# Optimization experiments

Hardware: AMD Instinct MI355X
Metric: run time of the kernel (lower is better)

The kernel has to match this reference:

```python
import jax, jax.numpy as jnp
import numpy as np

IN_DIM, HIDDEN_DIM, OUT_DIM = 128, 256, 128
N_NODES, N_EDGES = 100000, 1000000


def setup_inputs() -> dict:
    key = jax.random.key(0)
    ks = jax.random.split(key, 8)
    s = lambda d: 1.0 / np.sqrt(d)
    x = jax.random.normal(ks[0], (N_NODES, IN_DIM), dtype=jnp.float32)
    edge_index = jax.random.randint(ks[1], (2, N_EDGES), 0, N_NODES, dtype=jnp.int64)
    # encoder: Linear(in,hid) -> ReLU -> Linear(hid,out)
    W1 = jax.random.uniform(ks[2], (IN_DIM, HIDDEN_DIM), jnp.float32, -s(IN_DIM), s(IN_DIM))
    b1 = jnp.zeros((HIDDEN_DIM,), jnp.float32)
    W2 = jax.random.uniform(ks[3], (HIDDEN_DIM, OUT_DIM), jnp.float32, -s(HIDDEN_DIM), s(HIDDEN_DIM))
    b2 = jnp.zeros((OUT_DIM,), jnp.float32)
    # pred: Linear(2*out,hid) -> ReLU -> Linear(hid,1)
    W3 = jax.random.uniform(ks[4], (2 * OUT_DIM, HIDDEN_DIM), jnp.float32, -s(2 * OUT_DIM), s(2 * OUT_DIM))
    b3 = jnp.zeros((HIDDEN_DIM,), jnp.float32)
    W4 = jax.random.uniform(ks[5], (HIDDEN_DIM, 1), jnp.float32, -s(HIDDEN_DIM), s(HIDDEN_DIM))
    b4 = jnp.zeros((1,), jnp.float32)
    return {"x": x, "edge_index": edge_index, "W1": W1, "b1": b1, "W2": W2,
            "b2": b2, "W3": W3, "b3": b3, "W4": W4, "b4": b4}


def reference(x, edge_index, W1, b1, W2, b2, W3, b3, W4, b4):
    # node encoder
    h = jax.nn.relu(x @ W1 + b1) @ W2 + b2            # [N, out_dim]
    # edge gather + concat
    h_src = h[edge_index[0]]                          # [E, out_dim]
    h_dst = h[edge_index[1]]                          # [E, out_dim]
    e = jnp.concatenate([h_src, h_dst], axis=-1)      # [E, 2*out_dim]
    # edge predictor
    logits = jax.nn.relu(e @ W3 + b3) @ W4 + b4       # [E, 1]
    return jax.nn.sigmoid(logits)
```

## Files before the change

### kernel.cpp

```cpp
#include <hip/hip_runtime.h>


#define NN 100000
#define NE 1000000
#define NTN 1563
#define GRID_N 256
#define GRID_EP 1024

typedef __attribute__((ext_vector_type(8))) __bf16 bf16x8;
typedef __attribute__((ext_vector_type(4))) float f32x4;
typedef __attribute__((ext_vector_type(4))) unsigned short us4;

__device__ __forceinline__ unsigned short f2bf(float f) {
    unsigned u = __float_as_uint(f);
    return (unsigned short)((u + 0x7FFFu + ((u >> 16) & 1u)) >> 16);
}
__device__ __forceinline__ float bflo(unsigned w) {
    return __uint_as_float(w << 16);
}
__device__ __forceinline__ float bfhi(unsigned w) {
    return __uint_as_float(w & 0xffff0000u);
}

template <int CTRL>
__device__ __forceinline__ float dpp_add(float v) {
    return v + __int_as_float(__builtin_amdgcn_update_dpp(
                   0, __float_as_int(v), CTRL, 0xF, 0xF, true));
}
__device__ __forceinline__ float row_reduce16(float v) {
    v = dpp_add<0x118>(v);
    v = dpp_add<0x114>(v);
    v = dpp_add<0x112>(v);
    v = dpp_add<0x111>(v);
    return v;
}

__global__ void prep1(const float* __restrict__ W1, const float* __restrict__ W2,
                      const float* __restrict__ W3, const float* __restrict__ b2,
                      const float* __restrict__ b3, const void* __restrict__ eidx,
                      unsigned short* __restrict__ w1s, float* __restrict__ wutf,
                      float* __restrict__ wvtf, float* __restrict__ bu,
                      float* __restrict__ bv, int* __restrict__ flag) {
    int t = blockIdx.x * blockDim.x + threadIdx.x;
    if (t < 32768) {
        int k = t >> 8, n = t & 255;
        w1s[(k >> 3) * 2048 + n * 8 + (k & 7)] = f2bf(W1[t]);
    }
    if (t < 65536) {
        int k = t >> 8, n = t & 255;
        float s = 0.0f;
        for (int j = 0; j < 128; ++j) s += W2[k * 128 + j] * W3[j * 256 + n];
        wutf[t] = s;
    } else {
        int i = t - 65536;
        int k = i >> 8, n = i & 255;
        float s = 0.0f;
        for (int j = 0; j < 128; ++j) s += W2[k * 128 + j] * W3[(128 + j) * 256 + n];
        wvtf[i] = s;
    }
    if (t < 256) {
        float s = b3[t];
        for (int j = 0; j < 128; ++j) s += b2[j] * W3[j * 256 + t];
        bu[t] = s;
    } else if (t < 512) {
        int n = t - 256;
        float s = 0.0f;
        for (int j = 0; j < 128; ++j) s += b2[j] * W3[(128 + j) * 256 + n];
        bv[n] = s;
    }
    if (t == 0) {
        const unsigned* u = (const unsigned*)eidx;
        int all0 = 1;
        for (int i = 0; i < 32; ++i) all0 &= (u[2 * i + 1] == 0u);
        *flag = all0;
    }
}

__global__ void prep2(const float* __restrict__ wutf, const float* __restrict__ wvtf,
                      unsigned short* __restrict__ wuts, unsigned short* __restrict__ wvts) {
    int t = blockIdx.x * blockDim.x + threadIdx.x;
    if (t < 65536) {
        int k = t >> 8, n = t & 255;
        wuts[(k >> 3) * 2048 + n * 8 + (k & 7)] = f2bf(wutf[t]);
    } else {
        int i = t - 65536;
        int k = i >> 8, n = i & 255;
        wvts[(k >> 3) * 2048 + n * 8 + (k & 7)] = f2bf(wvtf[i]);
    }
}

__global__ __launch_bounds__(512, 2) void node_uv(
    const float* __restrict__ x, const float* __restrict__ b1,
    const unsigned short* __restrict__ w1s, const unsigned short* __restrict__ wuts,
    const unsigned short* __restrict__ wvts, const float* __restrict__ bu,
    const float* __restrict__ bv, unsigned short* __restrict__ Ug,
    unsigned short* __restrict__ Vg) {
    __shared__ __align__(16) unsigned short A1[64 * 136];
    __shared__ __align__(16) unsigned short A2[64 * 264];

    const int t = threadIdx.x, lane = t & 63, w = t >> 6;
    const int cl = lane & 15, q = lane >> 4;
    const int nb = w * 32;

    bf16x8 wutr[8][2], wvtr[8][2];
#pragma unroll
    for (int s = 0; s < 8; ++s)
#pragma unroll
        for (int nt = 0; nt < 2; ++nt) {
            wutr[s][nt] = *(const bf16x8*)(wuts + (s * 4 + q) * 2048 +
                                           (nb + nt * 16 + cl) * 8);
            wvtr[s][nt] = *(const bf16x8*)(wvts + (s * 4 + q) * 2048 +
                                           (nb + nt * 16 + cl) * 8);
        }
    float b1v[2], buv[2], bvv[2];
#pragma unroll
    for (int nt = 0; nt < 2; ++nt) {
        int n = nb + nt * 16 + cl;
        b1v[nt] = b1[n];
        buv[nt] = bu[n];
        bvv[nt] = bv[n];
    }

    for (int tile = blockIdx.x; tile < NTN; tile += GRID_N) {
        const int m0 = tile * 64;
        {
            const float4* x4 = (const float4*)x;
#pragma unroll
            for (int i = 0; i < 4; ++i) {
                int lin = i * 512 + t;
                int m = lin >> 5, c = lin & 31;
                int node = m0 + m;
                if (node > NN - 1) node = NN - 1;
                float4 v = x4[node * 32 + c];
                us4 b;
                b.x = f2bf(v.x); b.y = f2bf(v.y); b.z = f2bf(v.z); b.w = f2bf(v.w);
                *(us4*)(A1 + m * 136 + c * 4) = b;
            }
        }
        __syncthreads();

        f32x4 acc[4][2];
#pragma unroll
        for (int mt = 0; mt < 4; ++mt)
#pragma unroll
            for (int nt = 0; nt < 2; ++nt)
                acc[mt][nt] = (f32x4){b1v[nt], b1v[nt], b1v[nt], b1v[nt]};
#pragma unroll
        for (int s = 0; s < 4; ++s) {
            bf16x8 a[4], bw[2];
#pragma unroll
            for (int mt = 0; mt < 4; ++mt)
                a[mt] = *(const bf16x8*)(A1 + (mt * 16 + cl) * 136 + s * 32 + q * 8);
#pragma unroll
            for (int nt = 0; nt < 2; ++nt)
                bw[nt] = *(const bf16x8*)(w1s + (s * 4 + q) * 2048 +
                                          (nb + nt * 16 + cl) * 8);
#pragma unroll
            for (int mt = 0; mt < 4; ++mt)
#pragma unroll
                for (int nt = 0; nt < 2; ++nt)
                    acc[mt][nt] = __builtin_amdgcn_mfma_f32_16x16x32_bf16(
                        a[mt], bw[nt], acc[mt][nt], 0, 0, 0);
        }
#pragma unroll
        for (int mt = 0; mt < 4; ++mt)
#pragma unroll
            for (int nt = 0; nt < 2; ++nt)
#pragma unroll
                for (int r = 0; r < 4; ++r) {
                    float v = fmaxf(acc[mt][nt][r], 0.0f);
                    A2[(mt * 16 + q * 4 + r) * 264 + nb + nt * 16 + cl] = f2bf(v);
                }
        __syncthreads();

        f32x4 accU[4][2], accV[4][2];
#pragma unroll
        for (int mt = 0; mt < 4; ++mt)
#pragma unroll
            for (int nt = 0; nt < 2; ++nt) {
                accU[mt][nt] = (f32x4){buv[nt], buv[nt], buv[nt], buv[nt]};
                accV[mt][nt] = (f32x4){bvv[nt], bvv[nt], bvv[nt], bvv[nt]};
            }
#pragma unroll
        for (int s = 0; s < 8; ++s) {
            bf16x8 a[4];
#pragma unroll
            for (int mt = 0; mt < 4; ++mt)
                a[mt] = *(const bf16x8*)(A2 + (mt * 16 + cl) * 264 + s * 32 + q * 8);
#pragma unroll
            for (int mt = 0; mt < 4; ++mt)
#pragma unroll
                for (int nt = 0; nt < 2; ++nt) {
                    accU[mt][nt] = __builtin_amdgcn_mfma_f32_16x16x32_bf16(
                        a[mt], wutr[s][nt], accU[mt][nt], 0, 0, 0);
                    accV[mt][nt] = __builtin_amdgcn_mfma_f32_16x16x32_bf16(
                        a[mt], wvtr[s][nt], accV[mt][nt], 0, 0, 0);
                }
        }
#pragma unroll
        for (int mt = 0; mt < 4; ++mt)
#pragma unroll
            for (int nt = 0; nt < 2; ++nt)
#pragma unroll
                for (int r = 0; r < 4; ++r) {
                    int node = m0 + mt * 16 + q * 4 + r;
                    if (node < NN) {
                        int col = nb + nt * 16 + cl;
                        Ug[node * 256 + col] = f2bf(accU[mt][nt][r]);
                        Vg[node * 256 + col] = f2bf(accV[mt][nt][r]);
                    }
                }
    }
}

#define TERM(uw, vw, wa, wb)                                     \
    (fmaxf(bflo(uw) + bflo(vw), 0.0f) * (wa) +                   \
     fmaxf(bfhi(uw) + bfhi(vw), 0.0f) * (wb))

__global__ __launch_bounds__(256, 4) void edge_pred(
    const void* __restrict__ eidx, const unsigned short* __restrict__ Ut,
    const unsigned short* __restrict__ Vt, const float* __restrict__ W4,
    const float* __restrict__ b4, const int* __restrict__ flag,
    float* __restrict__ out) {
    const int t = threadIdx.x, lane = t & 63;
    const int cl = lane & 15, g = lane >> 4;
    const int gwid = (blockIdx.x * 256 + t) >> 6;
    const int nw = (GRID_EP * 256) >> 6;
    const bool i64f = (*flag != 0);
    const int* ei32 = (const int*)eidx;
    const long long* ei64 = (const long long*)eidx;

    float w4a[8], w4b[8];
#pragma unroll
    for (int j = 0; j < 8; ++j) {
        w4a[j] = W4[cl * 8 + j];
        w4b[j] = W4[128 + cl * 8 + j];
    }
    const float b4v = b4[0];

    for (int base = gwid * 8; base < NE; base += nw * 8) {
        const int eA = base + g, eB = base + 4 + g;
        int sA = i64f ? (int)ei64[eA] : ei32[eA];
        int dA = i64f ? (int)ei64[NE + eA] : ei32[NE + eA];
        int sB = i64f ? (int)ei64[eB] : ei32[eB];
        int dB = i64f ? (int)ei64[NE + eB] : ei32[NE + eB];
        sA = sA < 0 ? 0 : (sA > NN - 1 ? NN - 1 : sA);
        dA = dA < 0 ? 0 : (dA > NN - 1 ? NN - 1 : dA);
        sB = sB < 0 ? 0 : (sB > NN - 1 ? NN - 1 : sB);
        dB = dB < 0 ? 0 : (dB > NN - 1 ? NN - 1 : dB);

        const uint4* ua = (const uint4*)(Ut + (long)sA * 256) + cl;
        const uint4* va = (const uint4*)(Vt + (long)dA * 256) + cl;
        const uint4* ub = (const uint4*)(Ut + (long)sB * 256) + cl;
        const uint4* vb = (const uint4*)(Vt + (long)dB * 256) + cl;
        uint4 ua0 = ua[0], ua1 = ua[16];
        uint4 va0 = va[0], va1 = va[16];
        uint4 ub0 = ub[0], ub1 = ub[16];
        uint4 vb0 = vb[0], vb1 = vb[16];

        float accA =
            TERM(ua0.x, va0.x, w4a[0], w4a[1]) + TERM(ua0.y, va0.y, w4a[2], w4a[3]) +
            TERM(ua0.z, va0.z, w4a[4], w4a[5]) + TERM(ua0.w, va0.w, w4a[6], w4a[7]) +
            TERM(ua1.x, va1.x, w4b[0], w4b[1]) + TERM(ua1.y, va1.y, w4b[2], w4b[3]) +
            TERM(ua1.z, va1.z, w4b[4], w4b[5]) + TERM(ua1.w, va1.w, w4b[6], w4b[7]);
        float accB =
            TERM(ub0.x, vb0.x, w4a[0], w4a[1]) + TERM(ub0.y, vb0.y, w4a[2], w4a[3]) +
            TERM(ub0.z, vb0.z, w4a[4], w4a[5]) + TERM(ub0.w, vb0.w, w4a[6], w4a[7]) +
            TERM(ub1.x, vb1.x, w4b[0], w4b[1]) + TERM(ub1.y, vb1.y, w4b[2], w4b[3]) +
            TERM(ub1.z, vb1.z, w4b[4], w4b[5]) + TERM(ub1.w, vb1.w, w4b[6], w4b[7]);

        accA = row_reduce16(accA);
        accB = row_reduce16(accB);
        if (cl == 15) {
            out[eA] = 1.0f / (1.0f + __expf(-(accA + b4v)));
            out[eB] = 1.0f / (1.0f + __expf(-(accB + b4v)));
        }
    }
}

extern "C" void kernel_launch(void* const* d_in, const int* in_sizes, int n_in,
                              void* d_out, int out_size, void* d_ws, size_t ws_size,
                              hipStream_t stream) {
    const float* x  = (const float*)d_in[0];
    const void*  ei = d_in[1];
    const float* W1 = (const float*)d_in[2];
    const float* b1 = (const float*)d_in[3];
    const float* W2 = (const float*)d_in[4];
    const float* b2 = (const float*)d_in[5];
    const float* W3 = (const float*)d_in[6];
    const float* b3 = (const float*)d_in[7];
    const float* W4 = (const float*)d_in[8];
    const float* b4 = (const float*)d_in[9];

    char* ws = (char*)d_ws;
    int* flag            = (int*)ws;
    unsigned short* w1s  = (unsigned short*)(ws + 256);
    unsigned short* wuts = (unsigned short*)(ws + 65792);
    unsigned short* wvts = (unsigned short*)(ws + 196864);
    float* bu            = (float*)(ws + 327936);
    float* bv            = (float*)(ws + 328960);
    float* wutf          = (float*)(ws + 329984);
    float* wvtf          = (float*)(ws + 592128);
    unsigned short* Ug   = (unsigned short*)(ws + 1048576);
    unsigned short* Vg   = (unsigned short*)(ws + 52248576);

    prep1<<<512, 256, 0, stream>>>(W1, W2, W3, b2, b3, ei, w1s, wutf, wvtf, bu, bv, flag);
    prep2<<<512, 256, 0, stream>>>(wutf, wvtf, wuts, wvts);
    node_uv<<<GRID_N, 512, 0, stream>>>(x, b1, w1s, wuts, wvts, bu, bv, Ug, Vg);
    edge_pred<<<GRID_EP, 256, 0, stream>>>(ei, Ug, Vg, W4, b4, flag, (float*)d_out);
}
```

Baseline: 328.1 us.

## Fuse weight prep kernels, use one-tile-per-block node encoder, enlarge edge grid

The prep2 kernel is merged into prep1 so the folded W2·W3 weights are written directly in bf16 swizzled layout, removing one launch and an fp32 round trip. node_uv moves from a persistent 256-block grid of 512 threads, which kept the U/V weights in registers, to one 64-node tile per 256-thread block. Each wave now covers 64 columns and the U and V GEMMs run in two sequential passes with weights streamed from global memory. The edge predictor grid is doubled and its launch bound raised to 8 blocks per CU for more occupancy, at the cost of register pressure and extra weight reloads per tile.

After: 331.8 us. No clear change (+1.1%).

```diff
diff --git a/kernel.cpp b/kernel.cpp
--- a/kernel.cpp
+++ b/kernel.cpp
@@ -4,8 +4,7 @@
 #define NN 100000
 #define NE 1000000
 #define NTN 1563
-#define GRID_N 256
-#define GRID_EP 1024
+#define GRID_EP 2048
 
 typedef __attribute__((ext_vector_type(8))) __bf16 bf16x8;
 typedef __attribute__((ext_vector_type(4))) float f32x4;
@@ -38,8 +37,9 @@
 __global__ void prep1(const float* __restrict__ W1, const float* __restrict__ W2,
                       const float* __restrict__ W3, const float* __restrict__ b2,
                       const float* __restrict__ b3, const void* __restrict__ eidx,
-                      unsigned short* __restrict__ w1s, float* __restrict__ wutf,
-                      float* __restrict__ wvtf, float* __restrict__ bu,
+                      unsigned short* __restrict__ w1s,
+                      unsigned short* __restrict__ wuts,
+                      unsigned short* __restrict__ wvts, float* __restrict__ bu,
                       float* __restrict__ bv, int* __restrict__ flag) {
     int t = blockIdx.x * blockDim.x + threadIdx.x;
     if (t < 32768) {
@@ -50,13 +50,13 @@
         int k = t >> 8, n = t & 255;
         float s = 0.0f;
         for (int j = 0; j < 128; ++j) s += W2[k * 128 + j] * W3[j * 256 + n];
-        wutf[t] = s;
+        wuts[(k >> 3) * 2048 + n * 8 + (k & 7)] = f2bf(s);
     } else {
         int i = t - 65536;
         int k = i >> 8, n = i & 255;
         float s = 0.0f;
         for (int j = 0; j < 128; ++j) s += W2[k * 128 + j] * W3[(128 + j) * 256 + n];
-        wvtf[i] = s;
+        wvts[(k >> 3) * 2048 + n * 8 + (k & 7)] = f2bf(s);
     }
     if (t < 256) {
         float s = b3[t];
@@ -76,20 +76,7 @@
     }
 }
 
-__global__ void prep2(const float* __restrict__ wutf, const float* __restrict__ wvtf,
-                      unsigned short* __restrict__ wuts, unsigned short* __restrict__ wvts) {
-    int t = blockIdx.x * blockDim.x + threadIdx.x;
-    if (t < 65536) {
-        int k = t >> 8, n = t & 255;
-        wuts[(k >> 3) * 2048 + n * 8 + (k & 7)] = f2bf(wutf[t]);
-    } else {
-        int i = t - 65536;
-        int k = i >> 8, n = i & 255;
-        wvts[(k >> 3) * 2048 + n * 8 + (k & 7)] = f2bf(wvtf[i]);
-    }
-}
-
-__global__ __launch_bounds__(512, 2) void node_uv(
+__global__ __launch_bounds__(256, 3) void node_uv(
     const float* __restrict__ x, const float* __restrict__ b1,
     const unsigned short* __restrict__ w1s, const unsigned short* __restrict__ wuts,
     const unsigned short* __restrict__ wvts, const float* __restrict__ bu,
@@ -100,115 +87,107 @@
 
     const int t = threadIdx.x, lane = t & 63, w = t >> 6;
     const int cl = lane & 15, q = lane >> 4;
-    const int nb = w * 32;
-
-    bf16x8 wutr[8][2], wvtr[8][2];
-#pragma unroll
-    for (int s = 0; s < 8; ++s)
-#pragma unroll
-        for (int nt = 0; nt < 2; ++nt) {
-            wutr[s][nt] = *(const bf16x8*)(wuts + (s * 4 + q) * 2048 +
-                                           (nb + nt * 16 + cl) * 8);
-            wvtr[s][nt] = *(const bf16x8*)(wvts + (s * 4 + q) * 2048 +
-                                           (nb + nt * 16 + cl) * 8);
-        }
-    float b1v[2], buv[2], bvv[2];
-#pragma unroll
-    for (int nt = 0; nt < 2; ++nt) {
+    const int nb = w * 64;
+    const int m0 = blockIdx.x * 64;
+
+    {
+        const float4* x4 = (const float4*)x;
+#pragma unroll
+        for (int i = 0; i < 8; ++i) {
+            int lin = i * 256 + t;
+            int m = lin >> 5, c = lin & 31;
+            int node = m0 + m;
+            if (node > NN - 1) node = NN - 1;
+            float4 v = x4[node * 32 + c];
+            us4 b;
+            b.x = f2bf(v.x); b.y = f2bf(v.y); b.z = f2bf(v.z); b.w = f2bf(v.w);
+            *(us4*)(A1 + m * 136 + c * 4) = b;
+        }
+    }
+    float b1v[4], buv[4], bvv[4];
+#pragma unroll
+    for (int nt = 0; nt < 4; ++nt) {
         int n = nb + nt * 16 + cl;
         b1v[nt] = b1[n];
         buv[nt] = bu[n];
         bvv[nt] = bv[n];
     }
-
-    for (int tile = blockIdx.x; tile < NTN; tile += GRID_N) {
-        const int m0 = tile * 64;
-        {
-            const float4* x4 = (const float4*)x;
-#pragma unroll
-            for (int i = 0; i < 4; ++i) {
-                int lin = i * 512 + t;
-                int m = lin >> 5, c = lin & 31;
-                int node = m0 + m;
-                if (node > NN - 1) node = NN - 1;
-                float4 v = x4[node * 32 + c];
-                us4 b;
-                b.x = f2bf(v.x); b.y = f2bf(v.y); b.z = f2bf(v.z); b.w = f2bf(v.w);
-                *(us4*)(A1 + m * 136 + c * 4) = b;
-            }
-        }
-        __syncthreads();
-
-        f32x4 acc[4][2];
-#pragma unroll
-        for (int mt = 0; mt < 4; ++mt)
-#pragma unroll
-            for (int nt = 0; nt < 2; ++nt)
+    __syncthreads();
+
+    {
+        f32x4 acc[4][4];
+#pragma unroll
+        for (int mt = 0; mt < 4; ++mt)
+#pragma unroll
+            for (int nt = 0; nt < 4; ++nt)
                 acc[mt][nt] = (f32x4){b1v[nt], b1v[nt], b1v[nt], b1v[nt]};
 #pragma unroll
         for (int s = 0; s < 4; ++s) {
-            bf16x8 a[4], bw[2];
+            bf16x8 a[4], bw[4];
 #pragma unroll
             for (int mt = 0; mt < 4; ++mt)
                 a[mt] = *(const bf16x8*)(A1 + (mt * 16 + cl) * 136 + s * 32 + q * 8);
 #pragma unroll
-            for (int nt = 0; nt < 2; ++nt)
+            for (int nt = 0; nt < 4; ++nt)
                 bw[nt] = *(const bf16x8*)(w1s + (s * 4 + q) * 2048 +
                                           (nb + nt * 16 + cl) * 8);
 #pragma unroll
             for (int mt = 0; mt < 4; ++mt)
 #pragma unroll
-                for (int nt = 0; nt < 2; ++nt)
+                for (int nt = 0; nt < 4; ++nt)
                     acc[mt][nt] = __builtin_amdgcn_mfma_f32_16x16x32_bf16(
                         a[mt], bw[nt], acc[mt][nt], 0, 0, 0);
         }
 #pragma unroll
         for (int mt = 0; mt < 4; ++mt)
 #pragma unroll
-            for (int nt = 0; nt < 2; ++nt)
+            for (int nt = 0; nt < 4; ++nt)
 #pragma unroll
                 for (int r = 0; r < 4; ++r) {
                     float v = fmaxf(acc[mt][nt][r], 0.0f);
                     A2[(mt * 16 + q * 4 + r) * 264 + nb + nt * 16 + cl] = f2bf(v);
                 }
-        __syncthreads();
-
-        f32x4 accU[4][2], accV[4][2];
-#pragma unroll
-        for (int mt = 0; mt < 4; ++mt)
-#pragma unroll
-            for (int nt = 0; nt < 2; ++nt) {
-                accU[mt][nt] = (f32x4){buv[nt], buv[nt], buv[nt], buv[nt]};
-                accV[mt][nt] = (f32x4){bvv[nt], bvv[nt], bvv[nt], bvv[nt]};
+    }
+    __syncthreads();
+
+#pragma unroll
+    for (int pass = 0; pass < 2; ++pass) {
+        const unsigned short* wt = pass ? wvts : wuts;
+        unsigned short* outg = pass ? Vg : Ug;
+        f32x4 acc[4][4];
+#pragma unroll
+        for (int mt = 0; mt < 4; ++mt)
+#pragma unroll
+            for (int nt = 0; nt < 4; ++nt) {
+                float bb = pass ? bvv[nt] : buv[nt];
+                acc[mt][nt] = (f32x4){bb, bb, bb, bb};
             }
 #pragma unroll
         for (int s = 0; s < 8; ++s) {
-            bf16x8 a[4];
+            bf16x8 a[4], bw[4];
 #pragma unroll
             for (int mt = 0; mt < 4; ++mt)
                 a[mt] = *(const bf16x8*)(A2 + (mt * 16 + cl) * 264 + s * 32 + q * 8);
 #pragma unroll
-            for (int mt = 0; mt < 4; ++mt)
-#pragma unroll
-                for (int nt = 0; nt < 2; ++nt) {
-                    accU[mt][nt] = __builtin_amdgcn_mfma_f32_16x16x32_bf16(
-                        a[mt], wutr[s][nt], accU[mt][nt], 0, 0, 0);
-                    accV[mt][nt] = __builtin_amdgcn_mfma_f32_16x16x32_bf16(
-                        a[mt], wvtr[s][nt], accV[mt][nt], 0, 0, 0);
-                }
-        }
-#pragma unroll
-        for (int mt = 0; mt < 4; ++mt)
-#pragma unroll
-            for (int nt = 0; nt < 2; ++nt)
+            for (int nt = 0; nt < 4; ++nt)
+                bw[nt] = *(const bf16x8*)(wt + (s * 4 + q) * 2048 +
+                                          (nb + nt * 16 + cl) * 8);
+#pragma unroll
+            for (int mt = 0; mt < 4; ++mt)
+#pragma unroll
+                for (int nt = 0; nt < 4; ++nt)
+                    acc[mt][nt] = __builtin_amdgcn_mfma_f32_16x16x32_bf16(
+                        a[mt], bw[nt], acc[mt][nt], 0, 0, 0);
+        }
+#pragma unroll
+        for (int mt = 0; mt < 4; ++mt)
+#pragma unroll
+            for (int nt = 0; nt < 4; ++nt)
 #pragma unroll
                 for (int r = 0; r < 4; ++r) {
                     int node = m0 + mt * 16 + q * 4 + r;
-                    if (node < NN) {
-                        int col = nb + nt * 16 + cl;
-                        Ug[node * 256 + col] = f2bf(accU[mt][nt][r]);
-                        Vg[node * 256 + col] = f2bf(accV[mt][nt][r]);
-                    }
+                    if (node < NN)
+                        outg[node * 256 + nb + nt * 16 + cl] = f2bf(acc[mt][nt][r]);
                 }
     }
 }
@@ -217,7 +196,7 @@
     (fmaxf(bflo(uw) + bflo(vw), 0.0f) * (wa) +                   \
      fmaxf(bfhi(uw) + bfhi(vw), 0.0f) * (wb))
 
-__global__ __launch_bounds__(256, 4) void edge_pred(
+__global__ __launch_bounds__(256, 8) void edge_pred(
     const void* __restrict__ eidx, const unsigned short* __restrict__ Ut,
     const unsigned short* __restrict__ Vt, const float* __restrict__ W4,
     const float* __restrict__ b4, const int* __restrict__ flag,
@@ -299,13 +278,10 @@
     unsigned short* wvts = (unsigned short*)(ws + 196864);
     float* bu            = (float*)(ws + 327936);
     float* bv            = (float*)(ws + 328960);
-    float* wutf          = (float*)(ws + 329984);
-    float* wvtf          = (float*)(ws + 592128);
     unsigned short* Ug   = (unsigned short*)(ws + 1048576);
     unsigned short* Vg   = (unsigned short*)(ws + 52248576);
 
-    prep1<<<512, 256, 0, stream>>>(W1, W2, W3, b2, b3, ei, w1s, wutf, wvtf, bu, bv, flag);
-    prep2<<<512, 256, 0, stream>>>(wutf, wvtf, wuts, wvts);
-    node_uv<<<GRID_N, 512, 0, stream>>>(x, b1, w1s, wuts, wvts, bu, bv, Ug, Vg);
+    prep1<<<512, 256, 0, stream>>>(W1, W2, W3, b2, b3, ei, w1s, wuts, wvts, bu, bv, flag);
+    node_uv<<<NTN, 256, 0, stream>>>(x, b1, w1s, wuts, wvts, bu, bv, Ug, Vg);
     edge_pred<<<GRID_EP, 256, 0, stream>>>(ei, Ug, Vg, W4, b4, flag, (float*)d_out);
 }
```
